# Kernel optimization log

Measured on AMD Instinct MI355X. Metric: run time of the kernel, lower is better.

Reference implementation:

```python
import jax, jax.numpy as jnp
import numpy as np

N, IN_FT, OUT_FT = 10000, 512, 256


def setup_inputs() -> dict:
    key = jax.random.key(0)
    k1, k2, k3 = jax.random.split(key, 3)
    feat = jax.random.normal(k1, (N, IN_FT), dtype=jnp.float32)
    adj = jax.random.uniform(k2, (N, N), dtype=jnp.float32)  # nonneg edge weights
    W = jax.random.normal(k3, (IN_FT, OUT_FT), dtype=jnp.float32) * 0.05
    conv_bias = jnp.zeros((OUT_FT,), dtype=jnp.float32)
    extra_bias = jnp.zeros((OUT_FT,), dtype=jnp.float32)
    return {"feat": feat, "adj": adj, "W": W,
            "conv_bias": conv_bias, "extra_bias": extra_bias}


def reference(feat, adj, W, conv_bias, extra_bias):
    n = adj.shape[0]
    idx = jnp.arange(n)
    # gcn_norm: fill_diag(adj, 1.0) -> self loops with weight 1 on the diagonal
    A_hat = adj.at[idx, idx].set(1.0)  # [N, N]
    deg = A_hat.sum(axis=1)            # row degree
    dinv = jnp.where(deg > 0, jax.lax.rsqrt(deg), 0.0)  # D^-1/2
    # linear transform first (standard GCNConv order), then normalized aggregation
    h = feat @ W                                   # [N, OUT_FT]
    # D^-1/2 A_hat D^-1/2 h, fused as row/col scalings to avoid a second NxN buffer
    agg = dinv[:, None] * (A_hat @ (dinv[:, None] * h))
    out = agg + conv_bias + extra_bias
    return jax.nn.relu(out)
```

## Files before the change

kernel.cpp:

```cpp
#include <hip/hip_runtime.h>

#define NROW 10000
#define NF 256
#define KF 512
#define MP 10048
#define NTILES 157

typedef __attribute__((ext_vector_type(8))) short short8x;
typedef __attribute__((ext_vector_type(4))) float f32x4;

__device__ __forceinline__ unsigned short bf16rne(float f){
  unsigned int u = __builtin_bit_cast(unsigned int, f);
  u += 0x7fffu + ((u >> 16) & 1u);
  return (unsigned short)(u >> 16);
}

__global__ void k_zero(float4* __restrict__ p){
  p[blockIdx.x * 256 + threadIdx.x] = make_float4(0.f, 0.f, 0.f, 0.f);
}

__global__ void k_deg(const float* __restrict__ adj, float* __restrict__ dinv){
  int i = blockIdx.x;
  int t = threadIdx.x;
  if (i >= NROW){ if (t == 0) dinv[i] = 0.f; return; }
  const float4* row = (const float4*)(adj + (size_t)i * NROW);
  float s = 0.f;
  for (int idx = t; idx < NROW/4; idx += 256){
    float4 v = row[idx];
    s += (v.x + v.y) + (v.z + v.w);
  }
  #pragma unroll
  for (int off = 32; off; off >>= 1) s += __shfl_down(s, off);
  __shared__ float red[4];
  if ((t & 63) == 0) red[t >> 6] = s;
  __syncthreads();
  if (t == 0){
    float tot = (red[0] + red[1]) + (red[2] + red[3]);
    float deg = tot - adj[(size_t)i * NROW + i] + 1.0f;
    dinv[i] = deg > 0.f ? rsqrtf(deg) : 0.f;
  }
}

__global__ __launch_bounds__(256) void k_featw(const float* __restrict__ feat,
        const float* __restrict__ W, const float* __restrict__ dinv,
        unsigned short* __restrict__ hsT){
  __shared__ __align__(16) float fs[32][512];
  int t = threadIdx.x;
  int i0 = blockIdx.x * 32;
  #pragma unroll
  for (int it = 0; it < 16; ++it){
    int e = it * 1024 + t * 4;
    int r = e >> 9, cc = e & 511;
    int gr = i0 + r; if (gr > NROW - 1) gr = NROW - 1;
    *(float4*)&fs[r][cc] = *(const float4*)(feat + (size_t)gr * KF + cc);
  }
  __syncthreads();
  float acc[32];
  #pragma unroll
  for (int r = 0; r < 32; ++r) acc[r] = 0.f;
  int c = t;
  for (int k = 0; k < KF; k += 4){
    float w0 = W[(k+0)*NF + c];
    float w1 = W[(k+1)*NF + c];
    float w2 = W[(k+2)*NF + c];
    float w3 = W[(k+3)*NF + c];
    #pragma unroll
    for (int r = 0; r < 32; ++r){
      float4 f = *(const float4*)&fs[r][k];
      acc[r] = fmaf(f.x, w0, acc[r]);
      acc[r] = fmaf(f.y, w1, acc[r]);
      acc[r] = fmaf(f.z, w2, acc[r]);
      acc[r] = fmaf(f.w, w3, acc[r]);
    }
  }
  unsigned short* dst = hsT + (size_t)c * MP + i0;
  #pragma unroll
  for (int r = 0; r < 32; r += 2){
    float a0 = acc[r]   * dinv[i0 + r];
    float a1 = acc[r+1] * dinv[i0 + r + 1];
    unsigned int u = (unsigned int)bf16rne(a0) | ((unsigned int)bf16rne(a1) << 16);
    *(unsigned int*)(dst + r) = u;
  }
}

__global__ __launch_bounds__(256, 2) void k_gemm(const float* __restrict__ adj,
        const unsigned short* __restrict__ hsT, float* __restrict__ out){
  __shared__ __align__(16) unsigned short Al[64][72];
  __shared__ __align__(16) unsigned short Bl[256][72];
  int t = threadIdx.x;
  int lane = t & 63, wid = t >> 6;
  int wr = wid >> 1, wc = wid & 1;
  int r0 = blockIdx.x * 64;
  int by = blockIdx.y;
  int kt0 = by * 39 + (by > 0 ? 1 : 0);
  int kt1 = (by + 1) * 39 + 1;

  f32x4 acc[2][8];
  #pragma unroll
  for (int a = 0; a < 2; ++a)
    #pragma unroll
    for (int b = 0; b < 8; ++b)
      #pragma unroll
      for (int j = 0; j < 4; ++j) acc[a][b][j] = 0.f;

  int arow = t >> 4;
  int acol = (t & 15) * 4;
  int bcol = t >> 3;
  int bko  = (t & 7) * 8;

  for (int kt = kt0; kt < kt1; ++kt){
    int k0 = kt * 64;
    #pragma unroll
    for (int it = 0; it < 4; ++it){
      int row = it * 16 + arow;
      int gr  = r0 + row;
      int gcb = k0 + acol;
      int er = gr  < NROW     ? gr  : NROW - 1;
      int ec = gcb <= NROW - 4 ? gcb : NROW - 4;
      float4 v = *(const float4*)(adj + (size_t)er * NROW + ec);
      float f0 = v.x, f1 = v.y, f2 = v.z, f3 = v.w;
      if (gr == gcb    ) f0 = 1.f;
      if (gr == gcb + 1) f1 = 1.f;
      if (gr == gcb + 2) f2 = 1.f;
      if (gr == gcb + 3) f3 = 1.f;
      unsigned int u0 = (unsigned int)bf16rne(f0) | ((unsigned int)bf16rne(f1) << 16);
      unsigned int u1 = (unsigned int)bf16rne(f2) | ((unsigned int)bf16rne(f3) << 16);
      *(uint2*)&Al[row][acol] = make_uint2(u0, u1);
    }
    #pragma unroll
    for (int it = 0; it < 8; ++it){
      int cc = it * 32 + bcol;
      *(uint4*)&Bl[cc][bko] = *(const uint4*)(hsT + (size_t)cc * MP + k0 + bko);
    }
    __syncthreads();
    #pragma unroll
    for (int kk = 0; kk < 64; kk += 32){
      short8x a0 = *(const short8x*)&Al[wr*32      + (lane & 15)][kk + (lane >> 4) * 8];
      short8x a1 = *(const short8x*)&Al[wr*32 + 16 + (lane & 15)][kk + (lane >> 4) * 8];
      #pragma unroll
      for (int ni = 0; ni < 8; ++ni){
        short8x b = *(const short8x*)&Bl[wc*128 + ni*16 + (lane & 15)][kk + (lane >> 4) * 8];
        acc[0][ni] = __builtin_amdgcn_mfma_f32_16x16x32_bf16(a0, b, acc[0][ni], 0, 0, 0);
        acc[1][ni] = __builtin_amdgcn_mfma_f32_16x16x32_bf16(a1, b, acc[1][ni], 0, 0, 0);
      }
    }
    __syncthreads();
  }
  #pragma unroll
  for (int mi = 0; mi < 2; ++mi){
    #pragma unroll
    for (int ni = 0; ni < 8; ++ni){
      int gc = wc*128 + ni*16 + (lane & 15);
      #pragma unroll
      for (int j = 0; j < 4; ++j){
        int gr = r0 + wr*32 + mi*16 + (lane >> 4) * 4 + j;
        if (gr < NROW) atomicAdd(out + (size_t)gr * NF + gc, acc[mi][ni][j]);
      }
    }
  }
}

__global__ void k_epi(float* __restrict__ out, const float* __restrict__ dinv,
                      const float* __restrict__ cb, const float* __restrict__ eb){
  int e = (blockIdx.x * 256 + threadIdx.x) * 4;
  int i = e >> 8, c = e & 255;
  float di = dinv[i];
  float4 v = *(float4*)(out + e);
  v.x = fmaxf(fmaf(v.x, di, cb[c+0] + eb[c+0]), 0.f);
  v.y = fmaxf(fmaf(v.y, di, cb[c+1] + eb[c+1]), 0.f);
  v.z = fmaxf(fmaf(v.z, di, cb[c+2] + eb[c+2]), 0.f);
  v.w = fmaxf(fmaf(v.w, di, cb[c+3] + eb[c+3]), 0.f);
  *(float4*)(out + e) = v;
}

extern "C" void kernel_launch(void* const* d_in, const int* in_sizes, int n_in,
                              void* d_out, int out_size, void* d_ws, size_t ws_size,
                              hipStream_t stream){
  const float* feat = (const float*)d_in[0];
  const float* adj  = (const float*)d_in[1];
  const float* W    = (const float*)d_in[2];
  const float* cb   = (const float*)d_in[3];
  const float* eb   = (const float*)d_in[4];
  float* out = (float*)d_out;

  float* dinv = (float*)d_ws;
  unsigned short* hsT = (unsigned short*)((char*)d_ws + 65536);

  k_zero <<<(NROW*NF)/1024, 256, 0, stream>>>((float4*)out);
  k_deg  <<<MP,            256, 0, stream>>>(adj, dinv);
  k_featw<<<MP/32,         256, 0, stream>>>(feat, W, dinv, hsT);
  k_gemm <<<dim3(NTILES,4),256, 0, stream>>>(adj, hsT, out);
  k_epi  <<<(NROW*NF)/1024,256, 0, stream>>>(out, dinv, cb, eb);
}
```

Baseline: 311.7 us.

## Fuse degree pass with adjacency bf16 pre-conversion and feature transform

After: 337.3 us. 1.08x slower.

```diff
diff --git a/kernel.cpp b/kernel.cpp
--- a/kernel.cpp
+++ b/kernel.cpp
@@ -5,6 +5,7 @@
 #define KF 512
 #define MP 10048
 #define NTILES 157
+#define RPB 16
 
 typedef __attribute__((ext_vector_type(8))) short short8x;
 typedef __attribute__((ext_vector_type(4))) float f32x4;
@@ -19,45 +20,61 @@
   p[blockIdx.x * 256 + threadIdx.x] = make_float4(0.f, 0.f, 0.f, 0.f);
 }
 
-__global__ void k_deg(const float* __restrict__ adj, float* __restrict__ dinv){
-  int i = blockIdx.x;
+__global__ __launch_bounds__(256) void k_pass1(const float* __restrict__ feat,
+        const float* __restrict__ adj, const float* __restrict__ W,
+        float* __restrict__ dinv, unsigned short* __restrict__ adjb,
+        unsigned short* __restrict__ hsT){
+  __shared__ __align__(16) float fs[RPB][512];
+  __shared__ float deg_part[RPB][4];
+  __shared__ float dinv_s[RPB];
   int t = threadIdx.x;
-  if (i >= NROW){ if (t == 0) dinv[i] = 0.f; return; }
-  const float4* row = (const float4*)(adj + (size_t)i * NROW);
-  float s = 0.f;
-  for (int idx = t; idx < NROW/4; idx += 256){
-    float4 v = row[idx];
-    s += (v.x + v.y) + (v.z + v.w);
-  }
-  #pragma unroll
-  for (int off = 32; off; off >>= 1) s += __shfl_down(s, off);
-  __shared__ float red[4];
-  if ((t & 63) == 0) red[t >> 6] = s;
+  int i0 = blockIdx.x * RPB;
+
+  #pragma unroll
+  for (int it = 0; it < (RPB*128)/256; ++it){
+    int idx = it * 256 + t;
+    int r = idx >> 7, c4 = (idx & 127) * 4;
+    *(float4*)&fs[r][c4] = *(const float4*)(feat + (size_t)(i0 + r) * KF + c4);
+  }
+
+  for (int r = 0; r < RPB; ++r){
+    int gr = i0 + r;
+    const float* src = adj  + (size_t)gr * NROW;
+    unsigned short* dst = adjb + (size_t)gr * MP;
+    float s = 0.f;
+    for (int idx = t; idx < MP/4; idx += 256){
+      int c = idx * 4;
+      uint2 o;
+      if (c < NROW){
+        float4 v = *(const float4*)(src + c);
+        if (gr == c    ) v.x = 1.f;
+        if (gr == c + 1) v.y = 1.f;
+        if (gr == c + 2) v.z = 1.f;
+        if (gr == c + 3) v.w = 1.f;
+        s += (v.x + v.y) + (v.z + v.w);
+        o.x = (unsigned int)bf16rne(v.x) | ((unsigned int)bf16rne(v.y) << 16);
+        o.y = (unsigned int)bf16rne(v.z) | ((unsigned int)bf16rne(v.w) << 16);
+      } else {
+        o = make_uint2(0u, 0u);
+      }
+      *(uint2*)(dst + c) = o;
+    }
+    #pragma unroll
+    for (int off = 32; off; off >>= 1) s += __shfl_down(s, off);
+    if ((t & 63) == 0) deg_part[r][t >> 6] = s;
+  }
   __syncthreads();
-  if (t == 0){
-    float tot = (red[0] + red[1]) + (red[2] + red[3]);
-    float deg = tot - adj[(size_t)i * NROW + i] + 1.0f;
-    dinv[i] = deg > 0.f ? rsqrtf(deg) : 0.f;
-  }
-}
-
-__global__ __launch_bounds__(256) void k_featw(const float* __restrict__ feat,
-        const float* __restrict__ W, const float* __restrict__ dinv,
-        unsigned short* __restrict__ hsT){
-  __shared__ __align__(16) float fs[32][512];
-  int t = threadIdx.x;
-  int i0 = blockIdx.x * 32;
-  #pragma unroll
-  for (int it = 0; it < 16; ++it){
-    int e = it * 1024 + t * 4;
-    int r = e >> 9, cc = e & 511;
-    int gr = i0 + r; if (gr > NROW - 1) gr = NROW - 1;
-    *(float4*)&fs[r][cc] = *(const float4*)(feat + (size_t)gr * KF + cc);
+  if (t < RPB){
+    float tot = (deg_part[t][0] + deg_part[t][1]) + (deg_part[t][2] + deg_part[t][3]);
+    float dv = tot > 0.f ? rsqrtf(tot) : 0.f;
+    dinv[i0 + t] = dv;
+    dinv_s[t] = dv;
   }
   __syncthreads();
-  float acc[32];
-  #pragma unroll
-  for (int r = 0; r < 32; ++r) acc[r] = 0.f;
+
+  float acc[RPB];
+  #pragma unroll
+  for (int r = 0; r < RPB; ++r) acc[r] = 0.f;
   int c = t;
   for (int k = 0; k < KF; k += 4){
     float w0 = W[(k+0)*NF + c];
@@ -65,7 +82,7 @@
     float w2 = W[(k+2)*NF + c];
     float w3 = W[(k+3)*NF + c];
     #pragma unroll
-    for (int r = 0; r < 32; ++r){
+    for (int r = 0; r < RPB; ++r){
       float4 f = *(const float4*)&fs[r][k];
       acc[r] = fmaf(f.x, w0, acc[r]);
       acc[r] = fmaf(f.y, w1, acc[r]);
@@ -73,17 +90,22 @@
       acc[r] = fmaf(f.w, w3, acc[r]);
     }
   }
-  unsigned short* dst = hsT + (size_t)c * MP + i0;
-  #pragma unroll
-  for (int r = 0; r < 32; r += 2){
-    float a0 = acc[r]   * dinv[i0 + r];
-    float a1 = acc[r+1] * dinv[i0 + r + 1];
+  unsigned short* hdst = hsT + (size_t)c * MP + i0;
+  #pragma unroll
+  for (int r = 0; r < RPB; r += 2){
+    float a0 = acc[r]   * dinv_s[r];
+    float a1 = acc[r+1] * dinv_s[r+1];
     unsigned int u = (unsigned int)bf16rne(a0) | ((unsigned int)bf16rne(a1) << 16);
-    *(unsigned int*)(dst + r) = u;
-  }
-}
-
-__global__ __launch_bounds__(256, 2) void k_gemm(const float* __restrict__ adj,
+    *(unsigned int*)(hdst + r) = u;
+  }
+  if (blockIdx.x == (NROW/RPB) - 1){
+    unsigned int* tz = (unsigned int*)(hsT + (size_t)t * MP + NROW);
+    #pragma unroll
+    for (int m = 0; m < (MP - NROW) / 2; ++m) tz[m] = 0u;
+  }
+}
+
+__global__ __launch_bounds__(256, 2) void k_gemm(const unsigned short* __restrict__ adjb,
         const unsigned short* __restrict__ hsT, float* __restrict__ out){
   __shared__ __align__(16) unsigned short Al[64][72];
   __shared__ __align__(16) unsigned short Bl[256][72];
@@ -103,29 +125,17 @@
       #pragma unroll
       for (int j = 0; j < 4; ++j) acc[a][b][j] = 0.f;
 
-  int arow = t >> 4;
-  int acol = (t & 15) * 4;
   int bcol = t >> 3;
   int bko  = (t & 7) * 8;
 
   for (int kt = kt0; kt < kt1; ++kt){
     int k0 = kt * 64;
     #pragma unroll
-    for (int it = 0; it < 4; ++it){
-      int row = it * 16 + arow;
-      int gr  = r0 + row;
-      int gcb = k0 + acol;
-      int er = gr  < NROW     ? gr  : NROW - 1;
-      int ec = gcb <= NROW - 4 ? gcb : NROW - 4;
-      float4 v = *(const float4*)(adj + (size_t)er * NROW + ec);
-      float f0 = v.x, f1 = v.y, f2 = v.z, f3 = v.w;
-      if (gr == gcb    ) f0 = 1.f;
-      if (gr == gcb + 1) f1 = 1.f;
-      if (gr == gcb + 2) f2 = 1.f;
-      if (gr == gcb + 3) f3 = 1.f;
-      unsigned int u0 = (unsigned int)bf16rne(f0) | ((unsigned int)bf16rne(f1) << 16);
-      unsigned int u1 = (unsigned int)bf16rne(f2) | ((unsigned int)bf16rne(f3) << 16);
-      *(uint2*)&Al[row][acol] = make_uint2(u0, u1);
+    for (int it = 0; it < 2; ++it){
+      int slot = it * 256 + t;
+      int row = slot >> 3, off8 = (slot & 7) * 8;
+      *(uint4*)&Al[row][off8] =
+          *(const uint4*)(adjb + (size_t)(r0 + row) * MP + k0 + off8);
     }
     #pragma unroll
     for (int it = 0; it < 8; ++it){
@@ -184,11 +194,11 @@
   float* out = (float*)d_out;
 
   float* dinv = (float*)d_ws;
-  unsigned short* hsT = (unsigned short*)((char*)d_ws + 65536);
-
-  k_zero <<<(NROW*NF)/1024, 256, 0, stream>>>((float4*)out);
-  k_deg  <<<MP,            256, 0, stream>>>(adj, dinv);
-  k_featw<<<MP/32,         256, 0, stream>>>(feat, W, dinv, hsT);
-  k_gemm <<<dim3(NTILES,4),256, 0, stream>>>(adj, hsT, out);
-  k_epi  <<<(NROW*NF)/1024,256, 0, stream>>>(out, dinv, cb, eb);
-}
+  unsigned short* hsT  = (unsigned short*)((char*)d_ws + (64u << 10));
+  unsigned short* adjb = (unsigned short*)((char*)d_ws + (8u << 20));
+
+  k_zero <<<(NROW*NF)/1024,  256, 0, stream>>>((float4*)out);
+  k_pass1<<<NROW/RPB,        256, 0, stream>>>(feat, adj, W, dinv, adjb, hsT);
+  k_gemm <<<dim3(NTILES, 4), 256, 0, stream>>>(adjb, hsT, out);
+  k_epi  <<<(NROW*NF)/1024,  256, 0, stream>>>(out, dinv, cb, eb);
+}
```

## Fuse degree pass with bf16 adjacency materialization and stream bf16 into GEMM

Applied to the files above, without the earlier changes.

Measured after the change: 357.4 us. 1.15x slower.

```diff
diff --git a/kernel.cpp b/kernel.cpp
--- a/kernel.cpp
+++ b/kernel.cpp
@@ -5,40 +5,66 @@
 #define KF 512
 #define MP 10048
 #define NTILES 157
+#define CCH 2512
 
 typedef __attribute__((ext_vector_type(8))) short short8x;
 typedef __attribute__((ext_vector_type(4))) float f32x4;
 
-__device__ __forceinline__ unsigned short bf16rne(float f){
+__device__ __forceinline__ unsigned int bf16rne(float f){
   unsigned int u = __builtin_bit_cast(unsigned int, f);
   u += 0x7fffu + ((u >> 16) & 1u);
-  return (unsigned short)(u >> 16);
+  return u >> 16;
 }
 
 __global__ void k_zero(float4* __restrict__ p){
   p[blockIdx.x * 256 + threadIdx.x] = make_float4(0.f, 0.f, 0.f, 0.f);
 }
 
-__global__ void k_deg(const float* __restrict__ adj, float* __restrict__ dinv){
-  int i = blockIdx.x;
+__global__ __launch_bounds__(256) void k_prep(const float* __restrict__ adj,
+        unsigned short* __restrict__ adjb, float* __restrict__ degp){
   int t = threadIdx.x;
-  if (i >= NROW){ if (t == 0) dinv[i] = 0.f; return; }
-  const float4* row = (const float4*)(adj + (size_t)i * NROW);
+  int lane = t & 63;
+  int row = blockIdx.x * 4 + (t >> 6);
+  int cy = blockIdx.y;
+  int c0 = cy * CCH;
+  const float* src = adj + (size_t)row * NROW + c0;
+  unsigned short* dst = adjb + (size_t)row * MP + c0;
   float s = 0.f;
-  for (int idx = t; idx < NROW/4; idx += 256){
-    float4 v = row[idx];
-    s += (v.x + v.y) + (v.z + v.w);
+  #pragma unroll
+  for (int it = 0; it < 10; ++it){
+    int idx = lane + it * 64;
+    if (idx < CCH/4){
+      int c4 = idx * 4;
+      int gc = c0 + c4;
+      float4 v = make_float4(0.f, 0.f, 0.f, 0.f);
+      if (gc < NROW){
+        v = *(const float4*)(src + c4);
+        if (row == gc    ) v.x = 1.f;
+        if (row == gc + 1) v.y = 1.f;
+        if (row == gc + 2) v.z = 1.f;
+        if (row == gc + 3) v.w = 1.f;
+        s += (v.x + v.y) + (v.z + v.w);
+      }
+      uint2 o;
+      o.x = bf16rne(v.x) | (bf16rne(v.y) << 16);
+      o.y = bf16rne(v.z) | (bf16rne(v.w) << 16);
+      *(uint2*)(dst + c4) = o;
+    }
   }
   #pragma unroll
   for (int off = 32; off; off >>= 1) s += __shfl_down(s, off);
-  __shared__ float red[4];
-  if ((t & 63) == 0) red[t >> 6] = s;
-  __syncthreads();
-  if (t == 0){
-    float tot = (red[0] + red[1]) + (red[2] + red[3]);
-    float deg = tot - adj[(size_t)i * NROW + i] + 1.0f;
-    dinv[i] = deg > 0.f ? rsqrtf(deg) : 0.f;
-  }
+  if (lane == 0) degp[cy * MP + row] = s;
+}
+
+__global__ void k_dinv(const float* __restrict__ degp, float* __restrict__ dinv){
+  int i = blockIdx.x * 256 + threadIdx.x;
+  if (i >= MP) return;
+  float d = 0.f;
+  if (i < NROW){
+    float tot = (degp[i] + degp[MP + i]) + (degp[2*MP + i] + degp[3*MP + i]);
+    d = tot > 0.f ? rsqrtf(tot) : 0.f;
+  }
+  dinv[i] = d;
 }
 
 __global__ __launch_bounds__(256) void k_featw(const float* __restrict__ feat,
@@ -78,12 +104,12 @@
   for (int r = 0; r < 32; r += 2){
     float a0 = acc[r]   * dinv[i0 + r];
     float a1 = acc[r+1] * dinv[i0 + r + 1];
-    unsigned int u = (unsigned int)bf16rne(a0) | ((unsigned int)bf16rne(a1) << 16);
+    unsigned int u = bf16rne(a0) | (bf16rne(a1) << 16);
     *(unsigned int*)(dst + r) = u;
   }
 }
 
-__global__ __launch_bounds__(256, 2) void k_gemm(const float* __restrict__ adj,
+__global__ __launch_bounds__(256, 2) void k_gemm(const unsigned short* __restrict__ adjb,
         const unsigned short* __restrict__ hsT, float* __restrict__ out){
   __shared__ __align__(16) unsigned short Al[64][72];
   __shared__ __align__(16) unsigned short Bl[256][72];
@@ -103,29 +129,17 @@
       #pragma unroll
       for (int j = 0; j < 4; ++j) acc[a][b][j] = 0.f;
 
-  int arow = t >> 4;
-  int acol = (t & 15) * 4;
   int bcol = t >> 3;
   int bko  = (t & 7) * 8;
 
   for (int kt = kt0; kt < kt1; ++kt){
     int k0 = kt * 64;
     #pragma unroll
-    for (int it = 0; it < 4; ++it){
-      int row = it * 16 + arow;
-      int gr  = r0 + row;
-      int gcb = k0 + acol;
-      int er = gr  < NROW     ? gr  : NROW - 1;
-      int ec = gcb <= NROW - 4 ? gcb : NROW - 4;
-      float4 v = *(const float4*)(adj + (size_t)er * NROW + ec);
-      float f0 = v.x, f1 = v.y, f2 = v.z, f3 = v.w;
-      if (gr == gcb    ) f0 = 1.f;
-      if (gr == gcb + 1) f1 = 1.f;
-      if (gr == gcb + 2) f2 = 1.f;
-      if (gr == gcb + 3) f3 = 1.f;
-      unsigned int u0 = (unsigned int)bf16rne(f0) | ((unsigned int)bf16rne(f1) << 16);
-      unsigned int u1 = (unsigned int)bf16rne(f2) | ((unsigned int)bf16rne(f3) << 16);
-      *(uint2*)&Al[row][acol] = make_uint2(u0, u1);
+    for (int it = 0; it < 2; ++it){
+      int slot = it * 256 + t;
+      int row = slot >> 3, off8 = (slot & 7) * 8;
+      *(uint4*)&Al[row][off8] =
+          *(const uint4*)(adjb + (size_t)(r0 + row) * MP + k0 + off8);
     }
     #pragma unroll
     for (int it = 0; it < 8; ++it){
@@ -183,12 +197,15 @@
   const float* eb   = (const float*)d_in[4];
   float* out = (float*)d_out;
 
-  float* dinv = (float*)d_ws;
-  unsigned short* hsT = (unsigned short*)((char*)d_ws + 65536);
-
-  k_zero <<<(NROW*NF)/1024, 256, 0, stream>>>((float4*)out);
-  k_deg  <<<MP,            256, 0, stream>>>(adj, dinv);
-  k_featw<<<MP/32,         256, 0, stream>>>(feat, W, dinv, hsT);
-  k_gemm <<<dim3(NTILES,4),256, 0, stream>>>(adj, hsT, out);
-  k_epi  <<<(NROW*NF)/1024,256, 0, stream>>>(out, dinv, cb, eb);
-}
+  float* degp = (float*)d_ws;
+  float* dinv = (float*)((char*)d_ws + (256u << 10));
+  unsigned short* hsT  = (unsigned short*)((char*)d_ws + (512u << 10));
+  unsigned short* adjb = (unsigned short*)((char*)d_ws + (8u << 20));
+
+  k_zero <<<(NROW*NF)/1024,    256, 0, stream>>>((float4*)out);
+  k_prep <<<dim3(NROW/4, 4),   256, 0, stream>>>(adj, adjb, degp);
+  k_dinv <<<(MP + 255)/256,    256, 0, stream>>>(degp, dinv);
+  k_featw<<<MP/32,             256, 0, stream>>>(feat, W, dinv, hsT);
+  k_gemm <<<dim3(NTILES, 4),   256, 0, stream>>>(adjb, hsT, out);
+  k_epi  <<<(NROW*NF)/1024,    256, 0, stream>>>(out, dinv, cb, eb);
+}
```
